# Performance work log

Measured on AMD Instinct MI355X. Metric: run time of the kernel, lower is better.

## Reference

```python
import jax, jax.numpy as jnp
import numpy as np
import math

ACCBLOCK = 32
SPLITS = 2


def _mam(x, w, accblock):
    """MAM fully-connected: block-accumulate products along K, then max+min over blocks.
    x: [M, K], w: [K, N]  ->  [M, N] = max_blk(partial) + min_blk(partial)
    Implemented as a scan over blocks with running max/min to avoid a [M, nblk, N] tensor.
    """
    M, K = x.shape
    N = w.shape[1]
    nblk = K // accblock
    assert nblk * accblock == K
    xb = x.reshape(M, nblk, accblock).transpose(1, 0, 2)  # [nblk, M, B]
    wb = w.reshape(nblk, accblock, N)                      # [nblk, B, N]
    big = jnp.asarray(jnp.finfo(x.dtype).max, x.dtype)

    def step(carry, blk):
        mx, mn = carry
        xi, wi = blk                      # [M, B], [B, N]
        s = xi @ wi                       # block partial sum [M, N]
        return (jnp.maximum(mx, s), jnp.minimum(mn, s)), None

    init = (jnp.full((M, N), -big, x.dtype), jnp.full((M, N), big, x.dtype))
    (mx, mn), _ = jax.lax.scan(step, init, (xb, wb))
    return mx + mn


def reference(x, weight, bias):
    # eval mode, vcon_steps=0 -> alpha=1, beta=0; no weight dropout, no output dropout
    in_features = weight.shape[1]
    w = weight.T  # [K, N]
    sub = math.ceil(in_features / SPLITS)
    last = in_features - sub * (SPLITS - 1)
    out = _mam(x[:, :sub], w[:sub], ACCBLOCK)
    for i in range(1, SPLITS - 1):
        out = out + _mam(x[:, i * sub:(i + 1) * sub], w[i * sub:(i + 1) * sub], ACCBLOCK)
    out = out + _mam(x[:, in_features - last:], w[in_features - last:], ACCBLOCK)
    return out + bias[None, :]


def setup_inputs() -> dict:
    key = jax.random.key(0)
    k1, k2, k3 = jax.random.split(key, 3)
    M, K, N = 2048, 4096, 4096
    x = jax.random.normal(k1, (M, K), dtype=jnp.float32)
    weight = jax.random.normal(k2, (N, K), dtype=jnp.float32) * (1.0 / math.sqrt(K))
    bias = jax.random.normal(k3, (N,), dtype=jnp.float32) * (1.0 / math.sqrt(K))
    return {"x": x, "weight": weight, "bias": bias}
```

## Files before the change

### kernel.cpp

```cpp
#include <hip/hip_runtime.h>
#include <cstdint>
#include <cstddef>

typedef __bf16 bf16;
typedef __bf16 bf16x4 __attribute__((ext_vector_type(4)));
typedef __bf16 bf16x8 __attribute__((ext_vector_type(8)));
typedef float  f32x4  __attribute__((ext_vector_type(4)));

#define MDIM 2048
#define NDIM 4096
#define KDIM 4096
#define FLOATMAX 3.402823466e38f

__global__ void cvt2_f32_to_bf16(const float* __restrict__ x, const float* __restrict__ w,
                                 bf16* __restrict__ xb, bf16* __restrict__ wb,
                                 int xn4, int wn4) {
    const int stride = gridDim.x * blockDim.x;
    int i = blockIdx.x * blockDim.x + threadIdx.x;
    for (int k = i; k < xn4; k += stride) {
        f32x4 v = reinterpret_cast<const f32x4*>(x)[k];
        reinterpret_cast<bf16x4*>(xb)[k] = __builtin_convertvector(v, bf16x4);
    }
    for (int k = i; k < wn4; k += stride) {
        f32x4 v = reinterpret_cast<const f32x4*>(w)[k];
        reinterpret_cast<bf16x4*>(wb)[k] = __builtin_convertvector(v, bf16x4);
    }
}

__device__ __forceinline__ void g2lds16(const bf16* g, bf16* l) {
    __builtin_amdgcn_global_load_lds(
        (const __attribute__((address_space(1))) uint32_t*)g,
        (__attribute__((address_space(3))) uint32_t*)l, 16, 0, 0);
}

__global__ __launch_bounds__(512, 2) void mam_kernel(
    const bf16* __restrict__ A,
    const bf16* __restrict__ B,
    const float* __restrict__ bias,
    float* __restrict__ out)
{
    __shared__ __align__(16) bf16 sA[2][2][128 * 32];
    __shared__ __align__(16) bf16 sB[2][2][128 * 32];

    const int t    = threadIdx.x;
    const int lane = t & 63;
    const int w    = t >> 6;
    const int wm   = (w >> 2) * 64;
    const int wn   = (w & 3) * 32;

    const int m0 = blockIdx.y * 128;
    const int n0 = blockIdx.x * 128;

    const int srow   = t >> 2;
    const int spos   = t & 3;
    const int schunk = spos ^ ((srow >> 1) & 3);
    const bf16* gA = A + (size_t)(m0 + srow) * KDIM + schunk * 8;
    const bf16* gB = B + (size_t)(n0 + srow) * KDIM + schunk * 8;
    const int ldst = t * 8;

    const int frow = lane & 15;
    const int q    = lane >> 4;
    int offA[4], offB[2];
#pragma unroll
    for (int i = 0; i < 4; ++i) {
        const int R = wm + i * 16 + frow;
        offA[i] = R * 32 + (q ^ ((R >> 1) & 3)) * 8;
    }
#pragma unroll
    for (int j = 0; j < 2; ++j) {
        const int R = wn + j * 16 + frow;
        offB[j] = R * 32 + (q ^ ((R >> 1) & 3)) * 8;
    }

    const f32x4 kZero = {0.f, 0.f, 0.f, 0.f};

    f32x4 acc[4][2], mx[4][2], mn[4][2];
#pragma unroll
    for (int i = 0; i < 4; ++i)
#pragma unroll
        for (int j = 0; j < 2; ++j) {
            acc[i][j] = kZero;
            mx[i][j] = (f32x4)(-FLOATMAX);
            mn[i][j] = (f32x4)(FLOATMAX);
        }

    auto prefetch = [&](int s, int pb) {
        const bf16* ga = gA + (size_t)s * 64;
        const bf16* gb = gB + (size_t)s * 64;
        g2lds16(ga,      &sA[pb][0][ldst]);
        g2lds16(ga + 32, &sA[pb][1][ldst]);
        g2lds16(gb,      &sB[pb][0][ldst]);
        g2lds16(gb + 32, &sB[pb][1][ldst]);
    };

    auto compute = [&](int pb) {
        bf16x8 aF0[4], aF1[4], bF0[2], bF1[2];
#pragma unroll
        for (int i = 0; i < 4; ++i) {
            aF0[i] = *(const bf16x8*)&sA[pb][0][offA[i]];
            aF1[i] = *(const bf16x8*)&sA[pb][1][offA[i]];
        }
#pragma unroll
        for (int j = 0; j < 2; ++j) {
            bF0[j] = *(const bf16x8*)&sB[pb][0][offB[j]];
            bF1[j] = *(const bf16x8*)&sB[pb][1][offB[j]];
        }
#pragma unroll
        for (int i = 0; i < 4; ++i) {
#pragma unroll
            for (int j = 0; j < 2; ++j) {
                f32x4 s0 = __builtin_amdgcn_mfma_f32_16x16x32_bf16(
                    aF0[i], bF0[j], kZero, 0, 0, 0);
                f32x4 s1 = __builtin_amdgcn_mfma_f32_16x16x32_bf16(
                    aF1[i], bF1[j], kZero, 0, 0, 0);
#pragma unroll
                for (int r = 0; r < 4; ++r) {
                    mx[i][j][r] = fmaxf(fmaxf(mx[i][j][r], s0[r]), s1[r]);
                    mn[i][j][r] = fminf(fminf(mn[i][j][r], s0[r]), s1[r]);
                }
            }
        }
    };

    auto split_reset = [&]() {
#pragma unroll
        for (int i = 0; i < 4; ++i)
#pragma unroll
            for (int j = 0; j < 2; ++j) {
                acc[i][j] += mx[i][j] + mn[i][j];
                mx[i][j] = (f32x4)(-FLOATMAX);
                mn[i][j] = (f32x4)(FLOATMAX);
            }
    };

    prefetch(0, 0);

    int bb = 0;
#pragma unroll 1
    for (int it = 0; it < 32; ++it) {
        __syncthreads();
        prefetch(bb + 1, 1);
        compute(0);
        ++bb;
        __syncthreads();
        if (bb < 63) prefetch(bb + 1, 0);
        compute(1);
        if (bb == 31 || bb == 63) split_reset();
        ++bb;
    }

    const int orow = (lane >> 4) * 4;
    const int ocol = lane & 15;
#pragma unroll
    for (int j = 0; j < 2; ++j) {
        const int col = n0 + wn + j * 16 + ocol;
        const float bv = bias[col];
#pragma unroll
        for (int i = 0; i < 4; ++i) {
            const int row = m0 + wm + i * 16 + orow;
#pragma unroll
            for (int r = 0; r < 4; ++r) {
                out[(size_t)(row + r) * NDIM + col] = acc[i][j][r] + bv;
            }
        }
    }
}

extern "C" void kernel_launch(void* const* d_in, const int* in_sizes, int n_in,
                              void* d_out, int out_size, void* d_ws, size_t ws_size,
                              hipStream_t stream) {
    const float* x    = (const float*)d_in[0];
    const float* wgt  = (const float*)d_in[1];
    const float* bias = (const float*)d_in[2];
    float* out = (float*)d_out;

    bf16* xbf = (bf16*)d_ws;
    bf16* wbf = xbf + (size_t)MDIM * KDIM;

    const int xn4 = (MDIM * KDIM) / 4;
    const int wn4 = (NDIM * KDIM) / 4;
    cvt2_f32_to_bf16<<<dim3(4096), dim3(256), 0, stream>>>(x, wgt, xbf, wbf, xn4, wn4);

    dim3 grid(NDIM / 128, MDIM / 128);
    mam_kernel<<<grid, dim3(512), 0, stream>>>(xbf, wbf, bias, out);
}
```

Measured before the change: 253.9 us.

## Split MAM K-halves across grid z with atomic output accumulation, 4-wave blocks

```diff
diff --git a/kernel.cpp b/kernel.cpp
--- a/kernel.cpp
+++ b/kernel.cpp
@@ -3,9 +3,9 @@
 #include <cstddef>
 
 typedef __bf16 bf16;
-typedef __bf16 bf16x4 __attribute__((ext_vector_type(4)));
 typedef __bf16 bf16x8 __attribute__((ext_vector_type(8)));
 typedef float  f32x4  __attribute__((ext_vector_type(4)));
+typedef float  f32x8  __attribute__((ext_vector_type(8)));
 
 #define MDIM 2048
 #define NDIM 4096
@@ -14,16 +14,20 @@
 
 __global__ void cvt2_f32_to_bf16(const float* __restrict__ x, const float* __restrict__ w,
                                  bf16* __restrict__ xb, bf16* __restrict__ wb,
-                                 int xn4, int wn4) {
+                                 int xn8, int wn8) {
     const int stride = gridDim.x * blockDim.x;
     int i = blockIdx.x * blockDim.x + threadIdx.x;
-    for (int k = i; k < xn4; k += stride) {
-        f32x4 v = reinterpret_cast<const f32x4*>(x)[k];
-        reinterpret_cast<bf16x4*>(xb)[k] = __builtin_convertvector(v, bf16x4);
+    for (int k = i; k < xn8; k += stride) {
+        f32x4 lo = reinterpret_cast<const f32x4*>(x)[2 * k];
+        f32x4 hi = reinterpret_cast<const f32x4*>(x)[2 * k + 1];
+        f32x8 v = {lo[0], lo[1], lo[2], lo[3], hi[0], hi[1], hi[2], hi[3]};
+        reinterpret_cast<bf16x8*>(xb)[k] = __builtin_convertvector(v, bf16x8);
     }
-    for (int k = i; k < wn4; k += stride) {
-        f32x4 v = reinterpret_cast<const f32x4*>(w)[k];
-        reinterpret_cast<bf16x4*>(wb)[k] = __builtin_convertvector(v, bf16x4);
+    for (int k = i; k < wn8; k += stride) {
+        f32x4 lo = reinterpret_cast<const f32x4*>(w)[2 * k];
+        f32x4 hi = reinterpret_cast<const f32x4*>(w)[2 * k + 1];
+        f32x8 v = {lo[0], lo[1], lo[2], lo[3], hi[0], hi[1], hi[2], hi[3]};
+        reinterpret_cast<bf16x8*>(wb)[k] = __builtin_convertvector(v, bf16x8);
     }
 }
 
@@ -33,7 +37,7 @@
         (__attribute__((address_space(3))) uint32_t*)l, 16, 0, 0);
 }
 
-__global__ __launch_bounds__(512, 2) void mam_kernel(
+__global__ __launch_bounds__(256, 2) void mam_kernel(
     const bf16* __restrict__ A,
     const bf16* __restrict__ B,
     const float* __restrict__ bias,
@@ -45,70 +49,73 @@
     const int t    = threadIdx.x;
     const int lane = t & 63;
     const int w    = t >> 6;
-    const int wm   = (w >> 2) * 64;
-    const int wn   = (w & 3) * 32;
+    const int wm   = (w >> 1) * 64;
+    const int wn   = (w & 1) * 64;
 
     const int m0 = blockIdx.y * 128;
     const int n0 = blockIdx.x * 128;
+    const int split = blockIdx.z;
+    const size_t kbase = (size_t)split * 2048;
 
-    const int srow   = t >> 2;
-    const int spos   = t & 3;
-    const int schunk = spos ^ ((srow >> 1) & 3);
-    const bf16* gA = A + (size_t)(m0 + srow) * KDIM + schunk * 8;
-    const bf16* gB = B + (size_t)(n0 + srow) * KDIM + schunk * 8;
-    const int ldst = t * 8;
+    const bf16* gAi[2];
+    const bf16* gBi[2];
+    int ldsOff[2];
+#pragma unroll
+    for (int i = 0; i < 2; ++i) {
+        const int r = i * 64 + (t >> 2);
+        const int p = t & 3;
+        const int c = p ^ ((r >> 1) & 3);
+        gAi[i] = A + (size_t)(m0 + r) * KDIM + kbase + c * 8;
+        gBi[i] = B + (size_t)(n0 + r) * KDIM + kbase + c * 8;
+        ldsOff[i] = (i * 256 + t) * 8;
+    }
 
     const int frow = lane & 15;
     const int q    = lane >> 4;
-    int offA[4], offB[2];
+    int offA[4], offB[4];
 #pragma unroll
     for (int i = 0; i < 4; ++i) {
-        const int R = wm + i * 16 + frow;
-        offA[i] = R * 32 + (q ^ ((R >> 1) & 3)) * 8;
-    }
-#pragma unroll
-    for (int j = 0; j < 2; ++j) {
-        const int R = wn + j * 16 + frow;
-        offB[j] = R * 32 + (q ^ ((R >> 1) & 3)) * 8;
+        const int RA = wm + i * 16 + frow;
+        offA[i] = RA * 32 + (q ^ ((RA >> 1) & 3)) * 8;
+        const int RB = wn + i * 16 + frow;
+        offB[i] = RB * 32 + (q ^ ((RB >> 1) & 3)) * 8;
     }
 
     const f32x4 kZero = {0.f, 0.f, 0.f, 0.f};
 
-    f32x4 acc[4][2], mx[4][2], mn[4][2];
+    f32x4 mx[4][4], mn[4][4];
 #pragma unroll
     for (int i = 0; i < 4; ++i)
 #pragma unroll
-        for (int j = 0; j < 2; ++j) {
-            acc[i][j] = kZero;
+        for (int j = 0; j < 4; ++j) {
             mx[i][j] = (f32x4)(-FLOATMAX);
             mn[i][j] = (f32x4)(FLOATMAX);
         }
 
     auto prefetch = [&](int s, int pb) {
-        const bf16* ga = gA + (size_t)s * 64;
-        const bf16* gb = gB + (size_t)s * 64;
-        g2lds16(ga,      &sA[pb][0][ldst]);
-        g2lds16(ga + 32, &sA[pb][1][ldst]);
-        g2lds16(gb,      &sB[pb][0][ldst]);
-        g2lds16(gb + 32, &sB[pb][1][ldst]);
+        const size_t so = (size_t)s * 64;
+#pragma unroll
+        for (int i = 0; i < 2; ++i) {
+            g2lds16(gAi[i] + so,      &sA[pb][0][ldsOff[i]]);
+            g2lds16(gAi[i] + so + 32, &sA[pb][1][ldsOff[i]]);
+            g2lds16(gBi[i] + so,      &sB[pb][0][ldsOff[i]]);
+            g2lds16(gBi[i] + so + 32, &sB[pb][1][ldsOff[i]]);
+        }
     };
 
     auto compute = [&](int pb) {
-        bf16x8 aF0[4], aF1[4], bF0[2], bF1[2];
+        bf16x8 aF0[4], aF1[4], bF0[4], bF1[4];
 #pragma unroll
         for (int i = 0; i < 4; ++i) {
             aF0[i] = *(const bf16x8*)&sA[pb][0][offA[i]];
             aF1[i] = *(const bf16x8*)&sA[pb][1][offA[i]];
-        }
-#pragma unroll
-        for (int j = 0; j < 2; ++j) {
-            bF0[j] = *(const bf16x8*)&sB[pb][0][offB[j]];
-            bF1[j] = *(const bf16x8*)&sB[pb][1][offB[j]];
+            bF0[i] = *(const bf16x8*)&sB[pb][0][offB[i]];
+            bF1[i] = *(const bf16x8*)&sB[pb][1][offB[i]];
         }
 #pragma unroll
         for (int i = 0; i < 4; ++i) {
 #pragma unroll
-            for (int j = 0; j < 2; ++j) {
+            for (int j = 0; j < 4; ++j) {
                 f32x4 s0 = __builtin_amdgcn_mfma_f32_16x16x32_bf16(
                     aF0[i], bF0[j], kZero, 0, 0, 0);
                 f32x4 s1 = __builtin_amdgcn_mfma_f32_16x16x32_bf16(
@@ -122,45 +129,31 @@
         }
     };
 
-    auto split_reset = [&]() {
-#pragma unroll
-        for (int i = 0; i < 4; ++i)
-#pragma unroll
-            for (int j = 0; j < 2; ++j) {
-                acc[i][j] += mx[i][j] + mn[i][j];
-                mx[i][j] = (f32x4)(-FLOATMAX);
-                mn[i][j] = (f32x4)(FLOATMAX);
-            }
-    };
-
     prefetch(0, 0);
 
-    int bb = 0;
 #pragma unroll 1
-    for (int it = 0; it < 32; ++it) {
+    for (int it = 0; it < 16; ++it) {
         __syncthreads();
-        prefetch(bb + 1, 1);
+        prefetch(2 * it + 1, 1);
         compute(0);
-        ++bb;
         __syncthreads();
-        if (bb < 63) prefetch(bb + 1, 0);
+        if (it < 15) prefetch(2 * it + 2, 0);
         compute(1);
-        if (bb == 31 || bb == 63) split_reset();
-        ++bb;
     }
 
     const int orow = (lane >> 4) * 4;
     const int ocol = lane & 15;
 #pragma unroll
-    for (int j = 0; j < 2; ++j) {
+    for (int j = 0; j < 4; ++j) {
         const int col = n0 + wn + j * 16 + ocol;
-        const float bv = bias[col];
+        const float bv = (split == 0) ? bias[col] : 0.0f;
 #pragma unroll
         for (int i = 0; i < 4; ++i) {
             const int row = m0 + wm + i * 16 + orow;
 #pragma unroll
             for (int r = 0; r < 4; ++r) {
-                out[(size_t)(row + r) * NDIM + col] = acc[i][j][r] + bv;
+                const float v = mx[i][j][r] + mn[i][j][r] + bv;
+                unsafeAtomicAdd(&out[(size_t)(row + r) * NDIM + col], v);
             }
         }
     }
@@ -177,10 +170,12 @@
     bf16* xbf = (bf16*)d_ws;
     bf16* wbf = xbf + (size_t)MDIM * KDIM;
 
-    const int xn4 = (MDIM * KDIM) / 4;
-    const int wn4 = (NDIM * KDIM) / 4;
-    cvt2_f32_to_bf16<<<dim3(4096), dim3(256), 0, stream>>>(x, wgt, xbf, wbf, xn4, wn4);
+    const int xn8 = (MDIM * KDIM) / 8;
+    const int wn8 = (NDIM * KDIM) / 8;
+    cvt2_f32_to_bf16<<<dim3(4096), dim3(256), 0, stream>>>(x, wgt, xbf, wbf, xn8, wn8);
 
-    dim3 grid(NDIM / 128, MDIM / 128);
-    mam_kernel<<<grid, dim3(512), 0, stream>>>(xbf, wbf, bias, out);
+    hipMemsetAsync(d_out, 0, (size_t)MDIM * NDIM * sizeof(float), stream);
+
+    dim3 grid(NDIM / 128, MDIM / 128, 2);
+    mam_kernel<<<grid, dim3(256), 0, stream>>>(xbf, wbf, bias, out);
 }
```

Result: slower. 497.9 us (+96.1%).
